# Performance work log

Measured on AMD Instinct MI355X. Metric: run time of the kernel, lower is better.

## Reference

```python
import jax, jax.numpy as jnp
import numpy as np

N_SENT = 100000   # source ('sent') nodes
N_TYPE = 10000    # destination ('type') nodes
E = 640000        # edges of etype 'has'
D = 128           # out_dim
LEAKY_SLOPE = 0.01  # F.leaky_relu default


def setup_inputs() -> dict:
    key = jax.random.key(0)
    k0, k1, k2, k3, k4 = jax.random.split(key, 5)
    h_sent = jax.random.normal(k0, (N_SENT, D), jnp.float32)
    h_type = jax.random.normal(k1, (N_TYPE, D), jnp.float32)
    # attn_fc: Linear(2*D, 1, bias=False) -> weight [1, 2*D]
    attn_w = jax.random.normal(k2, (1, 2 * D), jnp.float32) * (1.0 / np.sqrt(2 * D))
    src_idx = jax.random.randint(k3, (E,), 0, N_SENT, dtype=jnp.int32)
    dst_idx = jax.random.randint(k4, (E,), 0, N_TYPE, dtype=jnp.int32)
    return {"h_sent": h_sent, "h_type": h_type, "attn_w": attn_w,
            "src_idx": src_idx, "dst_idx": dst_idx}


def reference(h_sent, h_type, attn_w, src_idx, dst_idx):
    w = attn_w[0]  # [2D]
    # attn_fc(cat(src_h, dst_h)) == src_h @ w[:D] + dst_h @ w[D:]  (no bias)
    s_src = h_sent @ w[:D]   # [N_SENT]
    s_dst = h_type @ w[D:]   # [N_TYPE]
    e = jax.nn.leaky_relu(s_src[src_idx] + s_dst[dst_idx], LEAKY_SLOPE)  # [E]
    # segment (per-destination) softmax over incoming edges
    m = jax.ops.segment_max(e, dst_idx, num_segments=N_TYPE)             # [N_TYPE]
    m = jnp.where(jnp.isfinite(m), m, 0.0)                               # empty segments -> 0
    ex = jnp.exp(e - m[dst_idx])                                         # [E]
    denom = jax.ops.segment_sum(ex, dst_idx, num_segments=N_TYPE)        # [N_TYPE]
    alpha = ex / denom[dst_idx]                                          # [E]
    # weighted scatter-sum of source features into destination nodes
    msg = alpha[:, None] * h_sent[src_idx]                               # [E, D]
    h_new = jax.ops.segment_sum(msg, dst_idx, num_segments=N_TYPE)       # [N_TYPE, D]
    # DGL only updates nodes that received messages; isolated nodes keep h
    deg = jax.ops.segment_sum(jnp.ones_like(e), dst_idx, num_segments=N_TYPE)
    return jnp.where(deg[:, None] > 0, h_new, h_type)
```

## Files before the change

kernel.cpp:

```cpp
#include <hip/hip_runtime.h>
#include <stdint.h>
#include <stddef.h>

#define N_SENT 100000
#define N_TYPE 10000
#define NEDGE  640000
#define NROWS  (N_SENT + N_TYPE)
#define MAXDEG 256
#define HB     256
#define HCHUNK (NEDGE / HB)
#define NBUCK  4
#define BROWS  (N_SENT / NBUCK)

__device__ __forceinline__ float bf2f(uint32_t lo16) {
    return __builtin_bit_cast(float, lo16 << 16);
}
__device__ __forceinline__ uint32_t f2bf(float f) {
    uint32_t u = __builtin_bit_cast(uint32_t, f);
    return (u + 0x7fffu + ((u >> 16) & 1u)) >> 16;
}

__device__ __forceinline__ bool detect_bf16(const uint32_t* __restrict__ h) {
    uint32_t u = h[threadIdx.x & 63];
    uint32_t e_lo = (u >> 7) & 0xffu;
    int ok = (e_lo >= 100u && e_lo <= 140u) ? 1 : 0;
    unsigned long long m = __ballot(ok);
    return __popcll(m) >= 48;
}

#define SC_BLOCKS 6875

__global__ __launch_bounds__(256) void scores_k(const void* __restrict__ h_sent,
                                                const void* __restrict__ h_type,
                                                const void* __restrict__ attn_w,
                                                float* __restrict__ s_src,
                                                float* __restrict__ s_dst) {
    int t    = blockIdx.x * 256 + (int)threadIdx.x;
    int lane = threadIdx.x & 63;
    bool isbf = detect_bf16((const uint32_t*)h_sent);
    if (isbf) {
        uint4 wsv = ((const uint4*)attn_w)[lane & 15];
        uint4 wtv = ((const uint4*)attn_w)[16 + (lane & 15)];
        bool isSrc = t < N_SENT * 16;
        const uint4* p = isSrc ? (const uint4*)h_sent + t
                               : (const uint4*)h_type + (t - N_SENT * 16);
        uint4 h = *p;
        uint4 wv = isSrc ? wsv : wtv;
        float s = bf2f(h.x & 0xffffu) * bf2f(wv.x & 0xffffu)
                + bf2f(h.x >> 16)     * bf2f(wv.x >> 16)
                + bf2f(h.y & 0xffffu) * bf2f(wv.y & 0xffffu)
                + bf2f(h.y >> 16)     * bf2f(wv.y >> 16)
                + bf2f(h.z & 0xffffu) * bf2f(wv.z & 0xffffu)
                + bf2f(h.z >> 16)     * bf2f(wv.z >> 16)
                + bf2f(h.w & 0xffffu) * bf2f(wv.w & 0xffffu)
                + bf2f(h.w >> 16)     * bf2f(wv.w >> 16);
        s += __shfl_xor(s, 1, 64);
        s += __shfl_xor(s, 2, 64);
        s += __shfl_xor(s, 4, 64);
        s += __shfl_xor(s, 8, 64);
        if ((lane & 15) == 0) {
            int row = t >> 4;
            if (row < N_SENT) s_src[row] = s;
            else              s_dst[row - N_SENT] = s;
        }
    } else {
        float4 wsv = ((const float4*)attn_w)[lane & 31];
        float4 wtv = ((const float4*)attn_w)[32 + (lane & 31)];
        const int HALF = NROWS * 16;
        int it0 = t, it1 = t + HALF;
        bool s0 = it0 < N_SENT * 32, s1 = it1 < N_SENT * 32;
        const float4* p0 = s0 ? (const float4*)h_sent + it0
                              : (const float4*)h_type + (it0 - N_SENT * 32);
        const float4* p1 = s1 ? (const float4*)h_sent + it1
                              : (const float4*)h_type + (it1 - N_SENT * 32);
        float4 h0 = *p0;
        float4 h1 = *p1;
        __builtin_amdgcn_sched_barrier(0);
        float4 w0 = s0 ? wsv : wtv, w1 = s1 ? wsv : wtv;
        float a = h0.x * w0.x + h0.y * w0.y + h0.z * w0.z + h0.w * w0.w;
        float b = h1.x * w1.x + h1.y * w1.y + h1.z * w1.z + h1.w * w1.w;
        a += __shfl_xor(a, 1, 64);  b += __shfl_xor(b, 1, 64);
        a += __shfl_xor(a, 2, 64);  b += __shfl_xor(b, 2, 64);
        a += __shfl_xor(a, 4, 64);  b += __shfl_xor(b, 4, 64);
        a += __shfl_xor(a, 8, 64);  b += __shfl_xor(b, 8, 64);
        a += __shfl_xor(a, 16, 64); b += __shfl_xor(b, 16, 64);
        if ((lane & 31) == 0) {
            int r0 = it0 >> 5, r1 = it1 >> 5;
            if (r0 < N_SENT) s_src[r0] = a; else s_dst[r0 - N_SENT] = a;
            if (r1 < N_SENT) s_src[r1] = b; else s_dst[r1 - N_SENT] = b;
        }
    }
}

__global__ __launch_bounds__(256) void count_k(const int* __restrict__ dst,
                                               uint32_t* __restrict__ count2) {
    __shared__ uint32_t hist[N_TYPE];
    int cb = blockIdx.x;
    int t  = threadIdx.x;
#pragma unroll
    for (int i = 0; i < 40; i++) {
        int idx = i * 256 + t;
        if (idx < N_TYPE) hist[idx] = 0u;
    }
    __syncthreads();
    int e0 = cb * HCHUNK;
    int dv[10];
#pragma unroll
    for (int k = 0; k < 10; k++) {
        int i = k * 256 + t;
        dv[k] = dst[e0 + (i < HCHUNK ? i : HCHUNK - 1)];
    }
    __builtin_amdgcn_sched_barrier(0);
#pragma unroll
    for (int k = 0; k < 10; k++) {
        int i = k * 256 + t;
        if (i < HCHUNK) atomicAdd(&hist[dv[k]], 1u);
    }
    __syncthreads();
    uint4* row = (uint4*)(count2 + (size_t)cb * N_TYPE);
#pragma unroll
    for (int i = 0; i < 10; i++) {
        int idx = i * 256 + t;
        if (idx < N_TYPE / 4) row[idx] = ((const uint4*)hist)[idx];
    }
}

__global__ __launch_bounds__(256) void sumscan_k(uint32_t* __restrict__ count2,
                                                 uint32_t* __restrict__ total) {
    int tid  = blockIdx.x * 256 + (int)threadIdx.x;
    int lane = threadIdx.x & 63;
    int bin  = tid >> 3;
    int sub  = tid & 7;
    if (bin >= N_TYPE) return;
    uint32_t vals[32];
#pragma unroll
    for (int c = 0; c < 32; c++)
        vals[c] = count2[(size_t)(sub * 32 + c) * N_TYPE + bin];
    __builtin_amdgcn_sched_barrier(0);
    uint32_t lsum = 0;
#pragma unroll
    for (int c = 0; c < 32; c++) lsum += vals[c];
    uint32_t incl = lsum;
#pragma unroll
    for (int off = 1; off < 8; off <<= 1) {
        uint32_t v = __shfl_up(incl, off, 64);
        if ((lane & 7) >= off) incl += v;
    }
    uint32_t run = incl - lsum;
#pragma unroll
    for (int c = 0; c < 32; c++) {
        uint32_t v = vals[c];
        count2[(size_t)(sub * 32 + c) * N_TYPE + bin] = run;
        run += v;
    }
    if (sub == 7) total[bin] = incl;
}

__global__ __launch_bounds__(1024) void scan_k(const uint32_t* __restrict__ total,
                                               uint32_t* __restrict__ offsets) {
    const int CH = 10;
    int t = threadIdx.x, lane = t & 63, wv = t >> 6;
    int base = t * CH;
    uint32_t local[CH];
    uint32_t tsum = 0;
#pragma unroll
    for (int i = 0; i < CH; i++) {
        int idx = base + i;
        uint32_t c = (idx < N_TYPE) ? total[idx] : 0u;
        local[i] = c;
        tsum += c;
    }
    uint32_t orig = tsum;
#pragma unroll
    for (int off = 1; off < 64; off <<= 1) {
        uint32_t v = __shfl_up(tsum, off, 64);
        if (lane >= off) tsum += v;
    }
    __shared__ uint32_t wsum[16];
    if (lane == 63) wsum[wv] = tsum;
    __syncthreads();
    if (wv == 0 && lane < 16) {
        uint32_t u = wsum[lane], o = u;
#pragma unroll
        for (int off = 1; off < 16; off <<= 1) {
            uint32_t v = __shfl_up(u, off, 64);
            if (lane >= off) u += v;
        }
        wsum[lane] = u - o;
    }
    __syncthreads();
    uint32_t run = wsum[wv] + tsum - orig;
#pragma unroll
    for (int i = 0; i < CH; i++) {
        int idx = base + i;
        if (idx < N_TYPE) {
            offsets[idx] = run;
            run += local[i];
        } else if (idx == N_TYPE) {
            offsets[idx] = run;
        }
    }
}

__global__ __launch_bounds__(256) void fill_k(const int* __restrict__ src,
                                              const int* __restrict__ dst,
                                              const uint32_t* __restrict__ offsets,
                                              const uint32_t* __restrict__ base2,
                                              uint32_t* __restrict__ edge_src) {
    __shared__ uint32_t cur[N_TYPE];
    int cb = blockIdx.x;
    int t  = threadIdx.x;
    const uint32_t* brow = base2 + (size_t)cb * N_TYPE;
#pragma unroll
    for (int i = 0; i < 10; i++) {
        int idx = i * 256 + t;
        if (idx < N_TYPE / 4) {
            uint4 o = ((const uint4*)offsets)[idx];
            uint4 b = ((const uint4*)brow)[idx];
            uint4 c; c.x = o.x + b.x; c.y = o.y + b.y; c.z = o.z + b.z; c.w = o.w + b.w;
            ((uint4*)cur)[idx] = c;
        }
    }
    __syncthreads();
    int e0 = cb * HCHUNK;
    int dv[10], sv[10];
#pragma unroll
    for (int k = 0; k < 10; k++) {
        int i = k * 256 + t;
        int e = e0 + (i < HCHUNK ? i : HCHUNK - 1);
        dv[k] = dst[e];
        sv[k] = src[e];
    }
    __builtin_amdgcn_sched_barrier(0);
#pragma unroll
    for (int k = 0; k < 10; k++) {
        int i = k * 256 + t;
        if (i < HCHUNK) {
            uint32_t pos = atomicAdd(&cur[dv[k]], 1u);
            edge_src[pos] = (uint32_t)sv[k];
        }
    }
}

__global__ __launch_bounds__(256) void pagg_k(const void* __restrict__ h_sent,
                                              const float* __restrict__ s_src,
                                              const float* __restrict__ s_dst,
                                              const uint32_t* __restrict__ offsets,
                                              const uint32_t* __restrict__ edge_src,
                                              float* __restrict__ part_m,
                                              float* __restrict__ part_d,
                                              uint32_t* __restrict__ part_v) {
    bool isbf = detect_bf16((const uint32_t*)h_sent);
    if (!isbf) return;
    __shared__ float    sc[4][MAXDEG];
    __shared__ uint32_t ss[4][MAXDEG];
    uint32_t p     = blockIdx.x & 3;
    int      wslot = threadIdx.x >> 6;
    int      lane  = threadIdx.x & 63;
    int      j     = (int)(blockIdx.x >> 2) * 4 + wslot;
    uint32_t beg = offsets[j];
    uint32_t deg = offsets[j + 1] - beg;
    float    sdj = s_dst[j];
    float*    mysc = sc[wslot];
    uint32_t* myss = ss[wslot];
    uint32_t pidx = (uint32_t)j * NBUCK + p;
    float m = -INFINITY;
    uint32_t cnt = 0;
    bool fits = deg <= MAXDEG;
    if (fits) {
        for (uint32_t k0 = 0; k0 < deg; k0 += 64) {
            uint32_t k = k0 + (uint32_t)lane;
            bool act = k < deg;
            uint32_t s = 0; float v = 0.0f; bool inb = false;
            if (act) {
                s = edge_src[beg + k];
                inb = (s / BROWS) == p;
                if (inb) {
                    v = s_src[s] + sdj;
                    v = v > 0.0f ? v : 0.01f * v;
                    m = fmaxf(m, v);
                }
            }
            unsigned long long msk = __ballot(inb ? 1 : 0);
            uint32_t pos = cnt + (uint32_t)__popcll(msk & ((1ull << lane) - 1ull));
            if (inb) { mysc[pos] = v; myss[pos] = s; }
            cnt += (uint32_t)__popcll(msk);
        }
    } else {
        for (uint32_t k = lane; k < deg; k += 64) {
            uint32_t s = edge_src[beg + k];
            if ((s / BROWS) == p) {
                float v = s_src[s] + sdj;
                v = v > 0.0f ? v : 0.01f * v;
                m = fmaxf(m, v);
            }
        }
    }
#pragma unroll
    for (int off = 32; off; off >>= 1) m = fmaxf(m, __shfl_xor(m, off, 64));
    if (m == -INFINITY) {
        if (lane == 0) part_d[pidx] = 0.0f;
        return;
    }
    float denom = 0.0f, a0 = 0.0f, a1 = 0.0f;
    const uint32_t* hp = (const uint32_t*)h_sent;
    if (fits) {
        uint32_t k = 0;
        for (; k + 8 <= cnt; k += 8) {
            uint32_t sv[8]; float vv[8]; uint32_t gv[8];
#pragma unroll
            for (int i = 0; i < 8; i++) { sv[i] = myss[k + i]; vv[i] = mysc[k + i]; }
#pragma unroll
            for (int i = 0; i < 8; i++) gv[i] = hp[(size_t)sv[i] * 64 + lane];
#pragma unroll
            for (int i = 0; i < 8; i++) {
                float w = __expf(vv[i] - m);
                denom += w;
                a0 += w * bf2f(gv[i] & 0xffffu);
                a1 += w * bf2f(gv[i] >> 16);
            }
        }
        for (; k < cnt; ++k) {
            float w = __expf(mysc[k] - m);
            uint32_t g = hp[(size_t)myss[k] * 64 + lane];
            denom += w;
            a0 += w * bf2f(g & 0xffffu);
            a1 += w * bf2f(g >> 16);
        }
    } else {
        for (uint32_t k = 0; k < deg; ++k) {
            uint32_t s = edge_src[beg + k];
            if ((s / BROWS) == p) {
                float v = s_src[s] + sdj; v = v > 0.0f ? v : 0.01f * v;
                float w = __expf(v - m);
                uint32_t g = hp[(size_t)s * 64 + lane];
                denom += w;
                a0 += w * bf2f(g & 0xffffu);
                a1 += w * bf2f(g >> 16);
            }
        }
    }
    if (lane == 0) { part_m[pidx] = m; part_d[pidx] = denom; }
    float inv = 1.0f / denom;
    uint32_t packed = f2bf(a0 * inv) | (f2bf(a1 * inv) << 16);
    __builtin_nontemporal_store(packed, part_v + (size_t)pidx * 64 + (size_t)lane);
}

__global__ __launch_bounds__(256) void pcomb_k(const void* __restrict__ h_sent,
                                               const void* __restrict__ h_type,
                                               const float* __restrict__ part_m,
                                               const float* __restrict__ part_d,
                                               const uint32_t* __restrict__ part_v,
                                               void* __restrict__ out) {
    bool isbf = detect_bf16((const uint32_t*)h_sent);
    if (!isbf) return;
    int j    = (blockIdx.x * 256 + (int)threadIdx.x) >> 6;
    int lane = threadIdx.x & 63;
    if (j >= N_TYPE) return;
    float dd[NBUCK], md[NBUCK];
#pragma unroll
    for (int p = 0; p < NBUCK; p++) dd[p] = part_d[j * NBUCK + p];
#pragma unroll
    for (int p = 0; p < NBUCK; p++) md[p] = part_m[j * NBUCK + p];
    float M = -INFINITY;
    bool any = false;
#pragma unroll
    for (int p = 0; p < NBUCK; p++)
        if (dd[p] > 0.0f) { M = fmaxf(M, md[p]); any = true; }
    if (!any) {
        ((uint32_t*)out)[(size_t)j * 64 + lane] =
            ((const uint32_t*)h_type)[(size_t)j * 64 + lane];
        return;
    }
    uint32_t gv[NBUCK];
#pragma unroll
    for (int p = 0; p < NBUCK; p++)
        gv[p] = __builtin_nontemporal_load(part_v + ((size_t)(j * NBUCK + p) * 64
                                                     + (size_t)lane));
    float D = 0.0f, a0 = 0.0f, a1 = 0.0f;
#pragma unroll
    for (int p = 0; p < NBUCK; p++) {
        bool ok = dd[p] > 0.0f;
        float W = ok ? dd[p] * __expf(md[p] - M) : 0.0f;
        D += W;
        a0 += W * (ok ? bf2f(gv[p] & 0xffffu) : 0.0f);
        a1 += W * (ok ? bf2f(gv[p] >> 16)     : 0.0f);
    }
    float inv = 1.0f / D;
    ((uint32_t*)out)[(size_t)j * 64 + lane] = f2bf(a0 * inv) | (f2bf(a1 * inv) << 16);
}

__global__ __launch_bounds__(256) void agg_k(const void* __restrict__ h_sent,
                                             const void* __restrict__ h_type,
                                             const float* __restrict__ s_src,
                                             const float* __restrict__ s_dst,
                                             const uint32_t* __restrict__ offsets,
                                             const uint32_t* __restrict__ edge_src,
                                             void* __restrict__ out,
                                             int use_part) {
    __shared__ float    sc[4][MAXDEG];
    __shared__ uint32_t ss[4][MAXDEG];
    bool isbf = detect_bf16((const uint32_t*)h_sent);
    if (use_part && isbf) return;
    int j     = (blockIdx.x * 256 + threadIdx.x) >> 6;
    int wslot = threadIdx.x >> 6;
    int lane  = threadIdx.x & 63;
    bool valid = j < N_TYPE;
    uint32_t beg = 0, deg = 0;
    float sdj = 0.0f;
    if (valid) {
        beg = offsets[j];
        deg = offsets[j + 1] - beg;
        sdj = s_dst[j];
    }
    float*    mysc = sc[wslot];
    uint32_t* myss = ss[wslot];
    bool fits = (deg <= MAXDEG);
    float m = -INFINITY;
    for (uint32_t k = lane; k < deg; k += 64) {
        uint32_t s = edge_src[beg + k];
        float v = s_src[s] + sdj;
        v = v > 0.0f ? v : 0.01f * v;
        if (fits) { mysc[k] = v; myss[k] = s; }
        m = fmaxf(m, v);
    }
#pragma unroll
    for (int off = 32; off; off >>= 1) m = fmaxf(m, __shfl_xor(m, off, 64));
    __syncthreads();
    if (!valid) return;
    if (deg == 0) {
        if (isbf) ((uint32_t*)out)[(size_t)j * 64 + lane] =
                      ((const uint32_t*)h_type)[(size_t)j * 64 + lane];
        else      ((float2*)out)[(size_t)j * 64 + lane] =
                      ((const float2*)h_type)[(size_t)j * 64 + lane];
        return;
    }
    float denom = 0.0f, a0 = 0.0f, a1 = 0.0f;
    if (isbf) {
        const uint32_t* hp = (const uint32_t*)h_sent;
        uint32_t k = 0;
        if (fits) {
            for (; k + 16 <= deg; k += 16) {
                uint32_t sv[16]; float vv[16]; uint32_t gv[16];
#pragma unroll
                for (int i = 0; i < 16; i++) { sv[i] = myss[k + i]; vv[i] = mysc[k + i]; }
#pragma unroll
                for (int i = 0; i < 16; i++) gv[i] = hp[(size_t)sv[i] * 64 + lane];
#pragma unroll
                for (int i = 0; i < 16; i++) {
                    float w = __expf(vv[i] - m);
                    denom += w;
                    a0 += w * bf2f(gv[i] & 0xffffu);
                    a1 += w * bf2f(gv[i] >> 16);
                }
            }
            for (; k + 8 <= deg; k += 8) {
                uint32_t sv[8]; float vv[8]; uint32_t gv[8];
#pragma unroll
                for (int i = 0; i < 8; i++) { sv[i] = myss[k + i]; vv[i] = mysc[k + i]; }
#pragma unroll
                for (int i = 0; i < 8; i++) gv[i] = hp[(size_t)sv[i] * 64 + lane];
#pragma unroll
                for (int i = 0; i < 8; i++) {
                    float w = __expf(vv[i] - m);
                    denom += w;
                    a0 += w * bf2f(gv[i] & 0xffffu);
                    a1 += w * bf2f(gv[i] >> 16);
                }
            }
            for (; k < deg; ++k) {
                float w = __expf(mysc[k] - m);
                uint32_t g = hp[(size_t)myss[k] * 64 + lane];
                denom += w;
                a0 += w * bf2f(g & 0xffffu);
                a1 += w * bf2f(g >> 16);
            }
        } else {
            for (k = 0; k < deg; ++k) {
                uint32_t s = edge_src[beg + k];
                float v = s_src[s] + sdj; v = v > 0.0f ? v : 0.01f * v;
                float w = __expf(v - m);
                uint32_t g = hp[(size_t)s * 64 + lane];
                denom += w;
                a0 += w * bf2f(g & 0xffffu);
                a1 += w * bf2f(g >> 16);
            }
        }
        float inv = 1.0f / denom;
        ((uint32_t*)out)[(size_t)j * 64 + lane] = f2bf(a0 * inv) | (f2bf(a1 * inv) << 16);
    } else {
        const float2* hp = (const float2*)h_sent;
        uint32_t k = 0;
        if (fits) {
            for (; k + 16 <= deg; k += 16) {
                uint32_t sv[16]; float vv[16]; float2 gv[16];
#pragma unroll
                for (int i = 0; i < 16; i++) { sv[i] = myss[k + i]; vv[i] = mysc[k + i]; }
#pragma unroll
                for (int i = 0; i < 16; i++) gv[i] = hp[(size_t)sv[i] * 64 + lane];
#pragma unroll
                for (int i = 0; i < 16; i++) {
                    float w = __expf(vv[i] - m);
                    denom += w;
                    a0 += w * gv[i].x;
                    a1 += w * gv[i].y;
                }
            }
            for (; k + 8 <= deg; k += 8) {
                uint32_t sv[8]; float vv[8]; float2 gv[8];
#pragma unroll
                for (int i = 0; i < 8; i++) { sv[i] = myss[k + i]; vv[i] = mysc[k + i]; }
#pragma unroll
                for (int i = 0; i < 8; i++) gv[i] = hp[(size_t)sv[i] * 64 + lane];
#pragma unroll
                for (int i = 0; i < 8; i++) {
                    float w = __expf(vv[i] - m);
                    denom += w;
                    a0 += w * gv[i].x;
                    a1 += w * gv[i].y;
                }
            }
            for (; k < deg; ++k) {
                float w = __expf(mysc[k] - m);
                float2 g = hp[(size_t)myss[k] * 64 + lane];
                denom += w;
                a0 += w * g.x;
                a1 += w * g.y;
            }
        } else {
            for (k = 0; k < deg; ++k) {
                uint32_t s = edge_src[beg + k];
                float v = s_src[s] + sdj; v = v > 0.0f ? v : 0.01f * v;
                float w = __expf(v - m);
                float2 g = hp[(size_t)s * 64 + lane];
                denom += w;
                a0 += w * g.x;
                a1 += w * g.y;
            }
        }
        float inv = 1.0f / denom;
        ((float2*)out)[(size_t)j * 64 + lane] = make_float2(a0 * inv, a1 * inv);
    }
}

static inline size_t align_up(size_t x) { return (x + 255) & ~(size_t)255; }

extern "C" void kernel_launch(void* const* d_in, const int* in_sizes, int n_in,
                              void* d_out, int out_size, void* d_ws, size_t ws_size,
                              hipStream_t stream) {
    const void* h_sent = d_in[0];
    const void* h_type = d_in[1];
    const void* attn_w = d_in[2];
    const int* src_idx = (const int*)d_in[3];
    const int* dst_idx = (const int*)d_in[4];

    char* w = (char*)d_ws;
    float*    s_src     = (float*)w;    w += align_up((size_t)N_SENT * 4);
    float*    s_dst     = (float*)w;    w += align_up((size_t)N_TYPE * 4);
    uint32_t* total     = (uint32_t*)w; w += align_up((size_t)N_TYPE * 4);
    uint32_t* offsets   = (uint32_t*)w; w += align_up((size_t)(N_TYPE + 1) * 4);
    uint32_t* edge_src  = (uint32_t*)w; w += align_up((size_t)NEDGE * 4);
    char* region = w;
    uint32_t* count2 = (uint32_t*)region;
    size_t count2_sz = align_up((size_t)HB * N_TYPE * 4);
    float*    part_m = (float*)region;
    float*    part_d = (float*)(region + align_up((size_t)N_TYPE * NBUCK * 4));
    uint32_t* part_v = (uint32_t*)(region + 2 * align_up((size_t)N_TYPE * NBUCK * 4));
    size_t part_sz = 2 * align_up((size_t)N_TYPE * NBUCK * 4)
                   + align_up((size_t)N_TYPE * NBUCK * 64 * 4);
    size_t base = (size_t)(region - (char*)d_ws);
    size_t region_sz = count2_sz > part_sz ? count2_sz : part_sz;
    int use_part = (base + region_sz <= ws_size) ? 1 : 0;

    scores_k<<<SC_BLOCKS, 256, 0, stream>>>(h_sent, h_type, attn_w, s_src, s_dst);
    count_k<<<HB, 256, 0, stream>>>(dst_idx, count2);
    sumscan_k<<<(N_TYPE * 8 + 255) / 256, 256, 0, stream>>>(count2, total);
    scan_k<<<1, 1024, 0, stream>>>(total, offsets);
    fill_k<<<HB, 256, 0, stream>>>(src_idx, dst_idx, offsets, count2, edge_src);
    if (use_part) {
        pagg_k<<<(N_TYPE / 4) * NBUCK, 256, 0, stream>>>(h_sent, s_src, s_dst,
                                                         offsets, edge_src,
                                                         part_m, part_d, part_v);
        pcomb_k<<<(N_TYPE + 3) / 4, 256, 0, stream>>>(h_sent, h_type,
                                                      part_m, part_d, part_v, d_out);
    }
    agg_k<<<(N_TYPE + 3) / 4, 256, 0, stream>>>(h_sent, h_type, s_src, s_dst,
                                                offsets, edge_src, d_out, use_part);
}
```

Measured before the change: 179.9 us.

## Use global max-score upper bound instead of per-segment max in partitioned softmax

The scores kernel now also reduces a global maximum of source scores through an order-preserving atomicMax. pagg_k uses leaky_relu(gmax + s_dst[j]) as a per-destination upper bound on the softmax shift. This drops the separate max pass and the per-bucket max/denominator partials, and the bucket denominators are accumulated with atomicAdd into dsum. pcomb_k then only sums the unnormalised partial vectors and divides by dsum. The trade-off is that the shift is no longer the true segment max, so exp values can underflow when scores in a segment sit far below the bound, and the partial vectors are stored unnormalised in bf16.

```diff
diff --git a/kernel.cpp b/kernel.cpp
--- a/kernel.cpp
+++ b/kernel.cpp
@@ -19,6 +19,14 @@
     uint32_t u = __builtin_bit_cast(uint32_t, f);
     return (u + 0x7fffu + ((u >> 16) & 1u)) >> 16;
 }
+__device__ __forceinline__ uint32_t encf(float f) {
+    uint32_t u = __builtin_bit_cast(uint32_t, f);
+    return (u >> 31) ? ~u : (u | 0x80000000u);
+}
+__device__ __forceinline__ float decf(uint32_t k) {
+    uint32_t u = (k >> 31) ? (k & 0x7fffffffu) : ~k;
+    return __builtin_bit_cast(float, u);
+}
 
 __device__ __forceinline__ bool detect_bf16(const uint32_t* __restrict__ h) {
     uint32_t u = h[threadIdx.x & 63];
@@ -34,7 +42,9 @@
                                                 const void* __restrict__ h_type,
                                                 const void* __restrict__ attn_w,
                                                 float* __restrict__ s_src,
-                                                float* __restrict__ s_dst) {
+                                                float* __restrict__ s_dst,
+                                                uint32_t* __restrict__ gmax) {
+    __shared__ float wmax[4];
     int t    = blockIdx.x * 256 + (int)threadIdx.x;
     int lane = threadIdx.x & 63;
     bool isbf = detect_bf16((const uint32_t*)h_sent);
@@ -63,6 +73,15 @@
             if (row < N_SENT) s_src[row] = s;
             else              s_dst[row - N_SENT] = s;
         }
+        float z = isSrc ? s : -INFINITY;
+        z = fmaxf(z, __shfl_xor(z, 16, 64));
+        z = fmaxf(z, __shfl_xor(z, 32, 64));
+        if (lane == 0) wmax[threadIdx.x >> 6] = z;
+        __syncthreads();
+        if (threadIdx.x == 0) {
+            float bm = fmaxf(fmaxf(wmax[0], wmax[1]), fmaxf(wmax[2], wmax[3]));
+            if (bm > -INFINITY) atomicMax(gmax, encf(bm));
+        }
     } else {
         float4 wsv = ((const float4*)attn_w)[lane & 31];
         float4 wtv = ((const float4*)attn_w)[32 + (lane & 31)];
@@ -245,10 +264,10 @@
 __global__ __launch_bounds__(256) void pagg_k(const void* __restrict__ h_sent,
                                               const float* __restrict__ s_src,
                                               const float* __restrict__ s_dst,
+                                              const uint32_t* __restrict__ gmax,
                                               const uint32_t* __restrict__ offsets,
                                               const uint32_t* __restrict__ edge_src,
-                                              float* __restrict__ part_m,
-                                              float* __restrict__ part_d,
+                                              float* __restrict__ dsum,
                                               uint32_t* __restrict__ part_v) {
     bool isbf = detect_bf16((const uint32_t*)h_sent);
     if (!isbf) return;
@@ -261,12 +280,15 @@
     uint32_t beg = offsets[j];
     uint32_t deg = offsets[j + 1] - beg;
     float    sdj = s_dst[j];
+    float    eb  = decf(*gmax) + sdj;
+    float    mj  = eb > 0.0f ? eb : 0.01f * eb;
     float*    mysc = sc[wslot];
     uint32_t* myss = ss[wslot];
     uint32_t pidx = (uint32_t)j * NBUCK + p;
-    float m = -INFINITY;
     uint32_t cnt = 0;
     bool fits = deg <= MAXDEG;
+    float denom = 0.0f, a0 = 0.0f, a1 = 0.0f;
+    const uint32_t* hp = (const uint32_t*)h_sent;
     if (fits) {
         for (uint32_t k0 = 0; k0 < deg; k0 += 64) {
             uint32_t k = k0 + (uint32_t)lane;
@@ -278,7 +300,6 @@
                 if (inb) {
                     v = s_src[s] + sdj;
                     v = v > 0.0f ? v : 0.01f * v;
-                    m = fmaxf(m, v);
                 }
             }
             unsigned long long msk = __ballot(inb ? 1 : 0);
@@ -286,25 +307,6 @@
             if (inb) { mysc[pos] = v; myss[pos] = s; }
             cnt += (uint32_t)__popcll(msk);
         }
-    } else {
-        for (uint32_t k = lane; k < deg; k += 64) {
-            uint32_t s = edge_src[beg + k];
-            if ((s / BROWS) == p) {
-                float v = s_src[s] + sdj;
-                v = v > 0.0f ? v : 0.01f * v;
-                m = fmaxf(m, v);
-            }
-        }
-    }
-#pragma unroll
-    for (int off = 32; off; off >>= 1) m = fmaxf(m, __shfl_xor(m, off, 64));
-    if (m == -INFINITY) {
-        if (lane == 0) part_d[pidx] = 0.0f;
-        return;
-    }
-    float denom = 0.0f, a0 = 0.0f, a1 = 0.0f;
-    const uint32_t* hp = (const uint32_t*)h_sent;
-    if (fits) {
         uint32_t k = 0;
         for (; k + 8 <= cnt; k += 8) {
             uint32_t sv[8]; float vv[8]; uint32_t gv[8];
@@ -314,14 +316,14 @@
             for (int i = 0; i < 8; i++) gv[i] = hp[(size_t)sv[i] * 64 + lane];
 #pragma unroll
             for (int i = 0; i < 8; i++) {
-                float w = __expf(vv[i] - m);
+                float w = __expf(vv[i] - mj);
                 denom += w;
                 a0 += w * bf2f(gv[i] & 0xffffu);
                 a1 += w * bf2f(gv[i] >> 16);
             }
         }
         for (; k < cnt; ++k) {
-            float w = __expf(mysc[k] - m);
+            float w = __expf(mysc[k] - mj);
             uint32_t g = hp[(size_t)myss[k] * 64 + lane];
             denom += w;
             a0 += w * bf2f(g & 0xffffu);
@@ -332,24 +334,23 @@
             uint32_t s = edge_src[beg + k];
             if ((s / BROWS) == p) {
                 float v = s_src[s] + sdj; v = v > 0.0f ? v : 0.01f * v;
-                float w = __expf(v - m);
+                float w = __expf(v - mj);
                 uint32_t g = hp[(size_t)s * 64 + lane];
                 denom += w;
                 a0 += w * bf2f(g & 0xffffu);
                 a1 += w * bf2f(g >> 16);
-            }
-        }
-    }
-    if (lane == 0) { part_m[pidx] = m; part_d[pidx] = denom; }
-    float inv = 1.0f / denom;
-    uint32_t packed = f2bf(a0 * inv) | (f2bf(a1 * inv) << 16);
+                cnt++;
+            }
+        }
+    }
+    if (lane == 0 && denom > 0.0f) atomicAdd(dsum + j, denom);
+    uint32_t packed = f2bf(a0) | (f2bf(a1) << 16);
     __builtin_nontemporal_store(packed, part_v + (size_t)pidx * 64 + (size_t)lane);
 }
 
 __global__ __launch_bounds__(256) void pcomb_k(const void* __restrict__ h_sent,
                                                const void* __restrict__ h_type,
-                                               const float* __restrict__ part_m,
-                                               const float* __restrict__ part_d,
+                                               const float* __restrict__ dsum,
                                                const uint32_t* __restrict__ part_v,
                                                void* __restrict__ out) {
     bool isbf = detect_bf16((const uint32_t*)h_sent);
@@ -357,17 +358,8 @@
     int j    = (blockIdx.x * 256 + (int)threadIdx.x) >> 6;
     int lane = threadIdx.x & 63;
     if (j >= N_TYPE) return;
-    float dd[NBUCK], md[NBUCK];
-#pragma unroll
-    for (int p = 0; p < NBUCK; p++) dd[p] = part_d[j * NBUCK + p];
-#pragma unroll
-    for (int p = 0; p < NBUCK; p++) md[p] = part_m[j * NBUCK + p];
-    float M = -INFINITY;
-    bool any = false;
-#pragma unroll
-    for (int p = 0; p < NBUCK; p++)
-        if (dd[p] > 0.0f) { M = fmaxf(M, md[p]); any = true; }
-    if (!any) {
+    float D = dsum[j];
+    if (!(D > 0.0f)) {
         ((uint32_t*)out)[(size_t)j * 64 + lane] =
             ((const uint32_t*)h_type)[(size_t)j * 64 + lane];
         return;
@@ -377,14 +369,11 @@
     for (int p = 0; p < NBUCK; p++)
         gv[p] = __builtin_nontemporal_load(part_v + ((size_t)(j * NBUCK + p) * 64
                                                      + (size_t)lane));
-    float D = 0.0f, a0 = 0.0f, a1 = 0.0f;
+    float a0 = 0.0f, a1 = 0.0f;
 #pragma unroll
     for (int p = 0; p < NBUCK; p++) {
-        bool ok = dd[p] > 0.0f;
-        float W = ok ? dd[p] * __expf(md[p] - M) : 0.0f;
-        D += W;
-        a0 += W * (ok ? bf2f(gv[p] & 0xffffu) : 0.0f);
-        a1 += W * (ok ? bf2f(gv[p] >> 16)     : 0.0f);
+        a0 += bf2f(gv[p] & 0xffffu);
+        a1 += bf2f(gv[p] >> 16);
     }
     float inv = 1.0f / D;
     ((uint32_t*)out)[(size_t)j * 64 + lane] = f2bf(a0 * inv) | (f2bf(a1 * inv) << 16);
@@ -557,32 +546,29 @@
     char* w = (char*)d_ws;
     float*    s_src     = (float*)w;    w += align_up((size_t)N_SENT * 4);
     float*    s_dst     = (float*)w;    w += align_up((size_t)N_TYPE * 4);
+    uint32_t* gmax      = (uint32_t*)((char*)s_dst + (size_t)N_TYPE * 4);
     uint32_t* total     = (uint32_t*)w; w += align_up((size_t)N_TYPE * 4);
     uint32_t* offsets   = (uint32_t*)w; w += align_up((size_t)(N_TYPE + 1) * 4);
     uint32_t* edge_src  = (uint32_t*)w; w += align_up((size_t)NEDGE * 4);
-    char* region = w;
-    uint32_t* count2 = (uint32_t*)region;
-    size_t count2_sz = align_up((size_t)HB * N_TYPE * 4);
-    float*    part_m = (float*)region;
-    float*    part_d = (float*)(region + align_up((size_t)N_TYPE * NBUCK * 4));
-    uint32_t* part_v = (uint32_t*)(region + 2 * align_up((size_t)N_TYPE * NBUCK * 4));
-    size_t part_sz = 2 * align_up((size_t)N_TYPE * NBUCK * 4)
-                   + align_up((size_t)N_TYPE * NBUCK * 64 * 4);
-    size_t base = (size_t)(region - (char*)d_ws);
-    size_t region_sz = count2_sz > part_sz ? count2_sz : part_sz;
-    int use_part = (base + region_sz <= ws_size) ? 1 : 0;
-
-    scores_k<<<SC_BLOCKS, 256, 0, stream>>>(h_sent, h_type, attn_w, s_src, s_dst);
+    uint32_t* count2    = (uint32_t*)w;
+    uint32_t* part_v    = (uint32_t*)w;
+    float*    dsum      = (float*)total;
+    size_t need = (size_t)(w - (char*)d_ws) + (size_t)HB * N_TYPE * 4;
+    int use_part = (need <= ws_size) ? 1 : 0;
+
+    hipMemsetAsync(gmax, 0, 4, stream);
+    scores_k<<<SC_BLOCKS, 256, 0, stream>>>(h_sent, h_type, attn_w, s_src, s_dst, gmax);
     count_k<<<HB, 256, 0, stream>>>(dst_idx, count2);
     sumscan_k<<<(N_TYPE * 8 + 255) / 256, 256, 0, stream>>>(count2, total);
     scan_k<<<1, 1024, 0, stream>>>(total, offsets);
     fill_k<<<HB, 256, 0, stream>>>(src_idx, dst_idx, offsets, count2, edge_src);
     if (use_part) {
-        pagg_k<<<(N_TYPE / 4) * NBUCK, 256, 0, stream>>>(h_sent, s_src, s_dst,
+        hipMemsetAsync(dsum, 0, (size_t)N_TYPE * 4, stream);
+        pagg_k<<<(N_TYPE / 4) * NBUCK, 256, 0, stream>>>(h_sent, s_src, s_dst, gmax,
                                                          offsets, edge_src,
-                                                         part_m, part_d, part_v);
+                                                         dsum, part_v);
         pcomb_k<<<(N_TYPE + 3) / 4, 256, 0, stream>>>(h_sent, h_type,
-                                                      part_m, part_d, part_v, d_out);
+                                                      dsum, part_v, d_out);
     }
     agg_k<<<(N_TYPE + 3) / 4, 256, 0, stream>>>(h_sent, h_type, s_src, s_dst,
                                                 offsets, edge_src, d_out, use_part);
```

Result: slower. 183.8 us (+2.2%).
